# Kernel optimization log

Hardware: AMD Instinct MI355X
Metric: run time of the kernel (lower is better)

## Reference

```python
import jax, jax.numpy as jnp
import numpy as np
import math


def ste_round(x):
    # round with straight-through gradient (identity in bwd)
    return x + jax.lax.stop_gradient(jnp.round(x) - x)


def ste_floor(x):
    return x + jax.lax.stop_gradient(jnp.floor(x) - x)


def _conv(x, w, b):
    # 5x5 stride-2 conv, padding=2 (kernel_size//2), NCHW/OIHW
    y = jax.lax.conv_general_dilated(
        x, w, window_strides=(2, 2), padding=[(2, 2), (2, 2)],
        dimension_numbers=('NCHW', 'OIHW', 'NCHW'))
    return y + b[None, :, None, None]


def _split_conv(x, w, b_int, mul, split=4):
    # 4 redundant sub-convolutions with floor-STE quantized integer weights/biases
    wq = ste_round(w)  # wSTE: round-to-int with STE
    out = 0.0
    for i in range(split):
        out = out + _conv(x, ste_floor((wq + i) / split), ste_floor((b_int + i) / split))
    return out * mul[None, :, None, None]


def _forward(x, w0, b0, w1, b1, w2, b2, w3, b3, mul0, mul1, mul2, mul3,
             relu0, relu1, relu2, md0, md1, md2, md3, ga_left):
    Bits = 8; clp_k = 8; in_scale = 8; scl_k = 3
    relus = [relu0, relu1, relu2]
    clp = [round((2 ** Bits - 1) / r * 2 ** (16 + clp_k)) for r in relus]
    scl = [math.floor((r + 2 ** (scl_k - 1)) / 2 ** scl_k) for r in relus]

    # quantize input to uint8 range
    x = jnp.clip(ste_round(x * 2 ** in_scale), 0, 255)

    # ---- layer 0 ----
    x = _split_conv(x, w0, ste_round(b0 * 2 ** in_scale), mul0)
    x = ste_floor((x + 2.0 ** (md0 - 1 + in_scale - clp_k)) / 2.0 ** (md0 + in_scale - clp_k))
    x = jnp.clip(x, 0, clp[0])
    x = ste_floor((ste_round(x * scl[0]) + 2.0 ** (15 + clp_k - scl_k)) / 2.0 ** (16 + clp_k - scl_k))

    # ---- layers 1, 2 ----
    for w_, b_, mul_, md_, idx in ((w1, b1, mul1, md1, 1), (w2, b2, mul2, md2, 2)):
        x = _split_conv(x, w_, ste_round(b_), mul_)
        x = ste_floor((x + 2.0 ** (md_ - 1 - clp_k)) / 2.0 ** (md_ - clp_k))
        x = jnp.clip(x, 0, clp[idx])
        x = ste_floor((ste_round(x * scl[idx]) + 2.0 ** (15 + clp_k - scl_k)) / 2.0 ** (16 + clp_k - scl_k))

    # ---- layer 3 (latent) ----
    x = _split_conv(x, w3, ste_round(b3), mul3)
    x = ste_floor((x + 2.0 ** (md3 - 1 - ga_left)) / 2.0 ** (md3 - ga_left))
    return x


def setup_inputs():
    key = jax.random.key(0)
    ks = jax.random.split(key, 16)
    N, M = 192, 320
    d = {}
    d['x'] = jax.random.uniform(ks[0], (4, 3, 512, 512), dtype=jnp.float32)
    # float weights whose round() gives small ints (integerized LIC weights)
    d['w0'] = jax.random.normal(ks[1], (N, 3, 5, 5), dtype=jnp.float32) * 3.0
    d['b0'] = jax.random.normal(ks[2], (N,), dtype=jnp.float32)
    d['w1'] = jax.random.normal(ks[3], (N, N, 5, 5), dtype=jnp.float32) * 3.0
    d['b1'] = jax.random.normal(ks[4], (N,), dtype=jnp.float32) * 16.0
    d['w2'] = jax.random.normal(ks[5], (N, N, 5, 5), dtype=jnp.float32) * 3.0
    d['b2'] = jax.random.normal(ks[6], (N,), dtype=jnp.float32) * 16.0
    d['w3'] = jax.random.normal(ks[7], (M, N, 5, 5), dtype=jnp.float32) * 3.0
    d['b3'] = jax.random.normal(ks[8], (M,), dtype=jnp.float32) * 16.0
    # per-channel integer-valued fixed-point multipliers
    d['mul0'] = jax.random.randint(ks[9], (N,), 1, 64).astype(jnp.float32)
    d['mul1'] = jax.random.randint(ks[10], (N,), 1, 64).astype(jnp.float32)
    d['mul2'] = jax.random.randint(ks[11], (N,), 1, 64).astype(jnp.float32)
    d['mul3'] = jax.random.randint(ks[12], (M,), 1, 64).astype(jnp.float32)
    d['relu0'] = 65536; d['relu1'] = 65536; d['relu2'] = 65536
    d['md0'] = 7; d['md1'] = 15; d['md2'] = 15; d['md3'] = 10
    d['ga_left'] = 4
    return d


def reference(x, w0, b0, w1, b1, w2, b2, w3, b3, mul0, mul1, mul2, mul3,
              relu0, relu1, relu2, md0, md1, md2, md3, ga_left):
    return _forward(x, w0, b0, w1, b1, w2, b2, w3, b3, mul0, mul1, mul2, mul3,
                    relu0, relu1, relu2, md0, md1, md2, md3, ga_left)
```

## Files before the change

### kernel.cpp

```cpp
#include <hip/hip_runtime.h>
#include <hip/hip_bf16.h>

typedef int i32x4 __attribute__((ext_vector_type(4)));
typedef unsigned int u32;
typedef unsigned long long u64;
typedef long long ll;

__device__ __forceinline__ void load_lds16(const void* g, void* l) {
  __builtin_amdgcn_global_load_lds(
      (const __attribute__((address_space(1))) u32*)g,
      (__attribute__((address_space(3))) u32*)l, 16, 0, 0);
}

__global__ __launch_bounds__(256) void prep_all(
    const float* __restrict__ w0, const float* __restrict__ w1,
    const float* __restrict__ w2, const float* __restrict__ w3,
    signed char* __restrict__ w0q, signed char* __restrict__ w1p,
    signed char* __restrict__ w2p, signed char* __restrict__ w3p,
    signed char* __restrict__ zbuf,
    int* __restrict__ totw0, int* __restrict__ totw1,
    int* __restrict__ totw2, int* __restrict__ totw3)
{
  __shared__ signed char ldsw[8 * 4800];
  const int blk = blockIdx.x;
  const int tid = threadIdx.x;

  if (blk < 88) {
    const float* wsrc; signed char* wdst; int* tot; int MF, sub;
    if (blk < 24)      { wsrc = w1; wdst = w1p; tot = totw1; MF = 12; sub = blk; }
    else if (blk < 48) { wsrc = w2; wdst = w2p; tot = totw2; MF = 12; sub = blk - 24; }
    else               { wsrc = w3; wdst = w3p; tot = totw3; MF = 20; sub = blk - 48; }
    const int mf = sub >> 1, half = sub & 1, colbase = half * 8;
    const int ocb = mf * 16 + colbase;
    for (int o = 0; o < 8; o++) {
      const float* src = wsrc + (size_t)(ocb + o) * 4800;
      int s = 0;
      for (int j = tid; j < 4800; j += 256) {
        int v = (int)rintf(src[j]);
        ldsw[o * 4800 + j] = (signed char)v;
        s += v;
      }
      atomicAdd(&tot[ocb + o], s);
    }
    __syncthreads();
    for (int u = tid; u < 9600; u += 256) {
      int eu = u & 3, colL = (u >> 2) & 7, q = (u >> 5) & 3, t = u >> 7;
      int tap = t / 3, ch = t - 3 * tap;
      int ci0 = ch * 64 + q * 16 + eu * 4;
      const signed char* sp = ldsw + colL * 4800 + tap;
      u32 wv = 0;
      #pragma unroll
      for (int bb = 0; bb < 4; bb++)
        wv |= ((u32)(unsigned char)sp[(ci0 + bb) * 25]) << (8 * bb);
      *(u32*)(wdst + ((size_t)t * MF + mf) * 1024 +
              (q * 16 + colbase + colL) * 16 + eu * 4) = wv;
    }
  } else {
    if (tid < 128) ((u64*)zbuf)[tid] = 0x8080808080808080ULL;
    for (int i = tid; i < 24576; i += 256) {
      int e = i & 15, colA = (i >> 4) & 15, q = (i >> 8) & 3, t = i >> 10;
      int mf = t % 12, ch = t / 12;
      signed char v = 0;
      if (e < 15 && (ch == 0 || q == 0)) {
        int ky = (ch == 0) ? q : 4;
        int ci = e / 5, kx = e - ci * 5;
        v = (signed char)(int)rintf(
            w0[((mf * 16 + colA) * 3 + ci) * 25 + ky * 5 + kx]);
      }
      w0q[i] = v;
    }
    for (int oc = tid; oc < 192; oc += 256) {
      const float* p = w0 + (size_t)oc * 75;
      int s = 0;
      #pragma unroll 5
      for (int j = 0; j < 75; j++) s += (int)rintf(p[j]);
      totw0[oc] = s;
    }
  }
}

__global__ __launch_bounds__(192, 3) void conv0F(
    const float* __restrict__ x, const signed char* __restrict__ wq,
    const float* __restrict__ bias, const float* __restrict__ mulv,
    const int* __restrict__ totw,
    const int* __restrict__ reluP, const int* __restrict__ mdP,
    unsigned char* __restrict__ outA)
{
  __shared__ signed char ilds[3][5][132];

  const int tid = threadIdx.x;
  const int lane = tid & 63;
  const int col = lane & 15;
  const int quad = lane >> 4;
  const int w = tid >> 6;
  const int blk = blockIdx.x;
  const int oxblk = blk & 3;
  const int oy = (blk >> 2) & 255;
  const int b = blk >> 10;
  const int oxbase = oxblk * 64;

  i32x4 afr[2][4];
  #pragma unroll
  for (int ch = 0; ch < 2; ch++)
    #pragma unroll
    for (int i = 0; i < 4; i++)
      afr[ch][i] = *(const i32x4*)(wq + ch * 12288 + (w * 4 + i) * 1024 + lane * 16);

  const float* xb = x + (size_t)b * 3 * 512 * 512;
  for (int i = tid; i < 990; i += 192) {
    int j = i % 66; int t = i / 66; int r = t % 5; int ci = t / 5;
    int iy = 2 * oy - 2 + r;
    int ix = 2 * oxbase - 2 + 2 * j;
    int v0 = -128, v1 = -128;
    if ((unsigned)iy < 512u) {
      const float* row = xb + ((size_t)ci * 512 + iy) * 512;
      if ((unsigned)ix < 512u) {
        float xv = rintf(row[ix] * 256.0f);
        v0 = (int)fminf(fmaxf(xv, 0.0f), 255.0f) - 128;
      }
      if ((unsigned)(ix + 1) < 512u) {
        float xv = rintf(row[ix + 1] * 256.0f);
        v1 = (int)fminf(fmaxf(xv, 0.0f), 255.0f) - 128;
      }
    }
    *(unsigned short*)&ilds[ci][r][2 * j] =
        (unsigned short)((v0 & 0xFF) | ((v1 & 0xFF) << 8));
  }
  __syncthreads();

  i32x4 acc[4][4];
  #pragma unroll
  for (int fm = 0; fm < 4; fm++)
    #pragma unroll
    for (int fn = 0; fn < 4; fn++) acc[fm][fn] = (i32x4){0, 0, 0, 0};

  #pragma unroll
  for (int ch = 0; ch < 2; ch++) {
    const int row = (ch == 0) ? quad : 4;
    i32x4 bfr[4];
    #pragma unroll
    for (int fn = 0; fn < 4; fn++) {
      const int xb2 = 2 * (fn * 16 + col);
      const int o8 = (xb2 & 3) * 8;
      const int ab = xb2 & ~3;
      u64 w0_, w1_, w2_;
      {
        const u32* p0 = (const u32*)&ilds[0][row][ab];
        const u32* p1 = (const u32*)&ilds[1][row][ab];
        const u32* p2 = (const u32*)&ilds[2][row][ab];
        w0_ = (u64)p0[0] | ((u64)p0[1] << 32);
        w1_ = (u64)p1[0] | ((u64)p1[1] << 32);
        w2_ = (u64)p2[0] | ((u64)p2[1] << 32);
      }
      u32 a0 = (u32)(w0_ >> o8);
      u32 a1 = ((u32)(w0_ >> (o8 + 32)) & 0xFFu) | (((u32)(w1_ >> o8)) << 8);
      u32 a2 = ((u32)(w1_ >> (o8 + 24)) & 0xFFFFu) | (((u32)(w2_ >> o8)) << 16);
      u32 a3 = (u32)(w2_ >> (o8 + 16));
      bfr[fn] = (i32x4){(int)a0, (int)a1, (int)a2, (int)a3};
    }
    #pragma unroll
    for (int fm = 0; fm < 4; fm++)
      #pragma unroll
      for (int fn = 0; fn < 4; fn++)
        acc[fm][fn] = __builtin_amdgcn_mfma_i32_16x16x64_i8(
            afr[ch][fm], bfr[fn], acc[fm][fn], 0, 0, 0);
  }

  const size_t pix0 = ((size_t)(b * 256 + oy)) * 256 + oxbase;
  const int rl = reluP[0];
  const int sh = mdP[0];
  const ll clpv_ll = llrint(255.0 / (double)rl * 16777216.0);
  const int clpv = clpv_ll > 0x7FFFFFFFLL ? 0x7FFFFFFF : (int)clpv_ll;
  const int sclv = (int)((rl + 4) >> 3);
  const int rnd = 1 << (sh - 1);
  #pragma unroll
  for (int fm = 0; fm < 4; fm++) {
    const int oc0 = w * 64 + fm * 16 + quad * 4;
    int bim[4], mu32[4];
    #pragma unroll
    for (int r = 0; r < 4; r++) {
      int bi = (int)llrintf(bias[oc0 + r] * 256.0f) + 128 * totw[oc0 + r];
      mu32[r] = (int)llrintf(mulv[oc0 + r]);
      bim[r] = bi * mu32[r];
    }
    #pragma unroll
    for (int fn = 0; fn < 4; fn++) {
      const size_t pix = pix0 + fn * 16 + col;
      u32 wd = 0;
      #pragma unroll
      for (int r = 0; r < 4; r++) {
        int vi = acc[fm][fn][r] * mu32[r] + bim[r];
        int y = (vi + rnd) >> sh;
        y = y < 0 ? 0 : (y > clpv ? clpv : y);
        y = (y * sclv + (1 << 20)) >> 21;
        wd |= (((u32)y ^ 0x80u) & 0xFFu) << (8 * r);
      }
      *(u32*)(outA + pix * 192 + oc0) = wd;
    }
  }
}

template <int COUT, int HIN, int WIN, int HOUT, int WOUT, int MW,
          int KSPLIT, bool DIRECT>
__global__ __launch_bounds__(MW * 64, 3) void convS(
    const signed char* __restrict__ act, const signed char* __restrict__ wp,
    const float* __restrict__ bias, const float* __restrict__ mulv,
    const int* __restrict__ totw,
    const int* __restrict__ reluP, const int* __restrict__ mdP,
    const signed char* __restrict__ zbuf,
    unsigned char* __restrict__ outA, int* __restrict__ outP)
{
  constexpr int CIN = 192;
  constexpr int PASSES = 4;
  constexpr int SAe = MW * 4096;
  constexpr int TX = WOUT / 16;
  constexpr int TYB = HOUT / 4;
  constexpr int TPP = 25 / KSPLIT;
  constexpr int NLOAD = PASSES * 3;
  constexpr int MAXL = (NLOAD + MW - 1) / MW;
  constexpr int BUF = NLOAD * 1024;
  constexpr int ROWSTEP = 2 * WIN * CIN;
  constexpr int PSZ = 4 * HOUT * WOUT * COUT;
  static_assert(MW * 64 == COUT, "M covers COUT");

  __shared__ __align__(16) char smem[2 * BUF];

  const int tid = threadIdx.x;
  const int lane = tid & 63;
  const int col = lane & 15;
  const int quad = lane >> 4;
  const int w = tid >> 6;
  const int part = blockIdx.y;

  int bx = blockIdx.x;
  const int tx = bx % TX; bx /= TX;
  const int ty = bx % TYB;
  const int b = bx / TYB;
  const int ox0 = tx * 16;
  const int oy0 = ty * 4;

  const signed char* base0 =
      act + ((size_t)b * HIN * WIN + (size_t)(2 * oy0) * WIN + 2 * (ox0 + col)) * CIN
      + quad * 16;
  int bmx = 0;
  #pragma unroll
  for (int kk = 0; kk < 5; kk++)
    if ((unsigned)(2 * (ox0 + col) + kk - 2) < (unsigned)WIN) bmx |= 1 << kk;
  int bmyPack = 0;
  #pragma unroll
  for (int p = 0; p < PASSES; p++) {
    #pragma unroll
    for (int kk = 0; kk < 5; kk++)
      if ((unsigned)(2 * (oy0 + p) + kk - 2) < (unsigned)HIN)
        bmyPack |= 1 << (p * 5 + kk);
  }

  const int tap0 = part * TPP;
  int kyS = tap0 / 5, kxS = tap0 - 5 * kyS;

  auto stage = [&](int sel) {
    const int offB = ((kyS - 2) * WIN + (kxS - 2)) * CIN;
    #pragma unroll
    for (int k = 0; k < MAXL; k++) {
      int j = w + k * MW;
      if (j >= NLOAD) break;
      int p = j / 3, c = j - 3 * p;
      bool v = ((bmx >> kxS) & 1) && ((bmyPack >> (p * 5 + kyS)) & 1);
      const signed char* g =
          v ? (base0 + (size_t)p * ROWSTEP + offB + c * 64) : (zbuf + quad * 16);
      load_lds16(g, smem + sel * BUF + j * 1024);
    }
    kxS++; if (kxS == 5) { kxS = 0; kyS++; }
  };

  i32x4 acc[4][4];
  #pragma unroll
  for (int fm = 0; fm < 4; fm++)
    #pragma unroll
    for (int fn = 0; fn < 4; fn++) acc[fm][fn] = (i32x4){0, 0, 0, 0};

  auto comp = [&](const char* pB, i32x4 (&a)[4]) {
    i32x4 bfr[4];
    #pragma unroll
    for (int i = 0; i < 4; i++)
      bfr[i] = *(const i32x4*)(pB + i * 3072);
    #pragma unroll
    for (int fm = 0; fm < 4; fm++)
      #pragma unroll
      for (int fn = 0; fn < 4; fn++)
        acc[fm][fn] = __builtin_amdgcn_mfma_i32_16x16x64_i8(
            a[fm], bfr[fn], acc[fm][fn], 0, 0, 0);
  };

  stage(0);
  const signed char* aptr = wp + (size_t)(tap0 * 3) * SAe + w * 4096 + lane * 16;
  i32x4 aC[4], aN[4];
  #pragma unroll
  for (int i = 0; i < 4; i++) aC[i] = *(const i32x4*)(aptr + i * 1024);

  #pragma unroll 1
  for (int t = 0; t < TPP; t++) {
    const int sel = t & 1;
    __syncthreads();
    if (t + 1 < TPP) stage(sel ^ 1);
    const char* base = smem + sel * BUF + lane * 16;
    #pragma unroll
    for (int c = 0; c < 3; c++) {
      aptr += SAe;
      #pragma unroll
      for (int i = 0; i < 4; i++) aN[i] = *(const i32x4*)(aptr + i * 1024);
      comp(base + c * 1024, aC);
      #pragma unroll
      for (int i = 0; i < 4; i++) aC[i] = aN[i];
    }
  }

  if constexpr (DIRECT) {
    const int rl = reluP[0];
    const int sh = mdP[0] - 8;
    const ll clpv = llrint(255.0 / (double)rl * 16777216.0);
    const ll sclv = (ll)((rl + 4) >> 3);
    #pragma unroll
    for (int fm = 0; fm < 4; fm++) {
      const int oc0 = w * 64 + fm * 16 + quad * 4;
      ll bi[4], mu[4];
      #pragma unroll
      for (int r = 0; r < 4; r++) {
        bi[r] = llrintf(bias[oc0 + r]) + 128LL * totw[oc0 + r];
        mu[r] = llrintf(mulv[oc0 + r]);
      }
      #pragma unroll
      for (int fn = 0; fn < 4; fn++) {
        const int oyv = oy0 + fn;
        const int oxv = ox0 + col;
        u32 wd = 0;
        #pragma unroll
        for (int r = 0; r < 4; r++) {
          ll vi = ((ll)acc[fm][fn][r] + bi[r]) * mu[r];
          ll y = (vi + (1LL << (sh - 1))) >> sh;
          y = y < 0 ? 0LL : (y > clpv ? clpv : y);
          y = (y * sclv + (1LL << 20)) >> 21;
          wd |= (((u32)y ^ 0x80u) & 0xFFu) << (8 * r);
        }
        *(u32*)(outA + ((size_t)((b * HOUT + oyv) * WOUT + oxv)) * COUT + oc0) = wd;
      }
    }
  } else {
    int* pout = outP + (size_t)part * PSZ;
    #pragma unroll
    for (int fm = 0; fm < 4; fm++) {
      const int oc0 = w * 64 + fm * 16 + quad * 4;
      #pragma unroll
      for (int fn = 0; fn < 4; fn++) {
        const int oyv = oy0 + fn;
        const int oxv = ox0 + col;
        *(i32x4*)(pout + ((size_t)((b * HOUT + oyv) * WOUT + oxv)) * COUT + oc0) =
            acc[fm][fn];
      }
    }
  }
}

__global__ __launch_bounds__(256) void reduce2(
    const int* __restrict__ partP, const float* __restrict__ bias,
    const float* __restrict__ mulv, const int* __restrict__ totw,
    const int* __restrict__ reluP, const int* __restrict__ mdP,
    unsigned char* __restrict__ outA)
{
  const int gid = blockIdx.x * 256 + threadIdx.x;
  const int PSZ4 = 4 * 64 * 64 * 192 / 4;
  const int4* pp = (const int4*)partP;
  int4 sv = pp[gid];
  #pragma unroll
  for (int p = 1; p < 5; p++) {
    int4 v = pp[(size_t)p * PSZ4 + gid];
    sv.x += v.x; sv.y += v.y; sv.z += v.z; sv.w += v.w;
  }
  int sa[4] = {sv.x, sv.y, sv.z, sv.w};
  const int oc0 = (gid * 4) % 192;
  const int rl = reluP[0];
  const int sh = mdP[0] - 8;
  const ll clpv = llrint(255.0 / (double)rl * 16777216.0);
  const ll sclv = (ll)((rl + 4) >> 3);
  u32 wd = 0;
  #pragma unroll
  for (int r = 0; r < 4; r++) {
    ll bi = llrintf(bias[oc0 + r]) + 128LL * totw[oc0 + r];
    ll mu = llrintf(mulv[oc0 + r]);
    ll vi = ((ll)sa[r] + bi) * mu;
    ll y = (vi + (1LL << (sh - 1))) >> sh;
    y = y < 0 ? 0LL : (y > clpv ? clpv : y);
    y = (y * sclv + (1LL << 20)) >> 21;
    wd |= (((u32)y ^ 0x80u) & 0xFFu) << (8 * r);
  }
  ((u32*)outA)[gid] = wd;
}

__global__ __launch_bounds__(256) void reduce3(
    const int* __restrict__ partP, const float* __restrict__ b3,
    const float* __restrict__ mul3, const int* __restrict__ totw3,
    const int* __restrict__ mdP, const int* __restrict__ gaP,
    float* __restrict__ outF)
{
  const int gid = blockIdx.x * 256 + threadIdx.x;
  int t = gid;
  const int ox = t & 31; t >>= 5;
  const int oy = t & 31; t >>= 5;
  const int oc = t % 320;
  const int b  = t / 320;
  const int PSZ = 4 * 32 * 32 * 320;
  const size_t src = ((size_t)((b * 32 + oy) * 32 + ox)) * 320 + oc;
  ll s = 0;
  #pragma unroll
  for (int p = 0; p < 5; p++) s += partP[(size_t)p * PSZ + src];
  const int sh = mdP[0] - gaP[0];
  const ll bi = llrintf(b3[oc]) + 128LL * totw3[oc];
  const ll mu = llrintf(mul3[oc]);
  const ll y = ((s + bi) * mu + (1LL << (sh - 1))) >> sh;
  outF[gid] = (float)y;
}

extern "C" void kernel_launch(void* const* d_in, const int* in_sizes, int n_in,
                              void* d_out, int out_size, void* d_ws, size_t ws_size,
                              hipStream_t stream)
{
  const float* x    = (const float*)d_in[0];
  const float* w0   = (const float*)d_in[1];
  const float* b0   = (const float*)d_in[2];
  const float* w1   = (const float*)d_in[3];
  const float* b1   = (const float*)d_in[4];
  const float* w2   = (const float*)d_in[5];
  const float* b2   = (const float*)d_in[6];
  const float* w3   = (const float*)d_in[7];
  const float* b3   = (const float*)d_in[8];
  const float* mul0 = (const float*)d_in[9];
  const float* mul1 = (const float*)d_in[10];
  const float* mul2 = (const float*)d_in[11];
  const float* mul3 = (const float*)d_in[12];
  const int* relu0  = (const int*)d_in[13];
  const int* relu1  = (const int*)d_in[14];
  const int* relu2  = (const int*)d_in[15];
  const int* md0    = (const int*)d_in[16];
  const int* md1    = (const int*)d_in[17];
  const int* md2    = (const int*)d_in[18];
  const int* md3    = (const int*)d_in[19];
  const int* ga     = (const int*)d_in[20];

  char* ws = (char*)d_ws;
  size_t off = 0;
  signed char* zbuf = (signed char*)(ws + off); off += 1024;
  signed char* w0q  = (signed char*)(ws + off); off += 24576;
  signed char* w1p  = (signed char*)(ws + off); off += 921600;
  signed char* w2p  = (signed char*)(ws + off); off += 921600;
  signed char* w3p  = (signed char*)(ws + off); off += 1536000;
  int*         totw1= (int*)        (ws + off); off += 192 * 4;
  int*         totw2= (int*)        (ws + off); off += 192 * 4;
  int*         totw3= (int*)        (ws + off); off += 320 * 4;
  int*         totw0= (int*)        (ws + off); off += 192 * 4;
  unsigned char* act1 = (unsigned char*)(ws + off); off += (size_t)4 * 256 * 256 * 192;
  unsigned char* act2 = (unsigned char*)(ws + off); off += (size_t)4 * 128 * 128 * 192;
  unsigned char* act3 = (unsigned char*)(ws + off); off += (size_t)4 * 64 * 64 * 192;
  int*         partl  = (int*)(ws + off); off += (size_t)5 * 4 * 64 * 64 * 192 * 4;
  (void)ws_size; (void)in_sizes; (void)n_in; (void)out_size;

  hipMemsetAsync(totw1, 0, (192 + 192 + 320 + 192) * 4, stream);
  prep_all<<<89, 256, 0, stream>>>(w0, w1, w2, w3, w0q, w1p, w2p, w3p,
                                   zbuf, totw0, totw1, totw2, totw3);
  conv0F<<<4096, 192, 0, stream>>>(x, w0q, b0, mul0, totw0, relu0, md0, act1);
  convS<192, 256, 256, 128, 128, 3, 1, true><<<dim3(1024, 1), 192, 0, stream>>>(
      (const signed char*)act1, w1p, b1, mul1, totw1, relu1, md1, zbuf, act2, nullptr);
  convS<192, 128, 128, 64, 64, 3, 5, false><<<dim3(256, 5), 192, 0, stream>>>(
      (const signed char*)act2, w2p, b2, mul2, totw2, relu2, md2, zbuf, nullptr, partl);
  reduce2<<<3072, 256, 0, stream>>>(partl, b2, mul2, totw2, relu2, md2, act3);
  convS<320, 64, 64, 32, 32, 5, 5, false><<<dim3(64, 5), 320, 0, stream>>>(
      (const signed char*)act3, w3p, b3, mul3, totw3, nullptr, md3, zbuf, nullptr, partl);
  reduce3<<<5120, 256, 0, stream>>>(partl, b3, mul3, totw3, md3, ga, (float*)d_out);
}
```

Before: 366.1 us.

## Stage whole input rows in swizzled LDS and reuse across kx taps

```diff
diff --git a/kernel.cpp b/kernel.cpp
--- a/kernel.cpp
+++ b/kernel.cpp
@@ -10,6 +10,10 @@
   __builtin_amdgcn_global_load_lds(
       (const __attribute__((address_space(1))) u32*)g,
       (__attribute__((address_space(3))) u32*)l, 16, 0, 0);
+}
+
+__device__ __forceinline__ int xcd_swz(int bid, int nwg) {
+  return (bid & 7) * (nwg >> 3) + (bid >> 3);
 }
 
 __global__ __launch_bounds__(256) void prep_all(
@@ -93,7 +97,7 @@
   const int col = lane & 15;
   const int quad = lane >> 4;
   const int w = tid >> 6;
-  const int blk = blockIdx.x;
+  const int blk = xcd_swz(blockIdx.x, gridDim.x);
   const int oxblk = blk & 3;
   const int oy = (blk >> 2) & 255;
   const int b = blk >> 10;
@@ -211,19 +215,15 @@
     unsigned char* __restrict__ outA, int* __restrict__ outP)
 {
   constexpr int CIN = 192;
-  constexpr int PASSES = 4;
   constexpr int SAe = MW * 4096;
   constexpr int TX = WOUT / 16;
   constexpr int TYB = HOUT / 4;
-  constexpr int TPP = 25 / KSPLIT;
-  constexpr int NLOAD = PASSES * 3;
-  constexpr int MAXL = (NLOAD + MW - 1) / MW;
-  constexpr int BUF = NLOAD * 1024;
-  constexpr int ROWSTEP = 2 * WIN * CIN;
+  constexpr int SLOTS = (KSPLIT == 1) ? 5 : 4;
+  constexpr int RS = 36 * 256;
   constexpr int PSZ = 4 * HOUT * WOUT * COUT;
   static_assert(MW * 64 == COUT, "M covers COUT");
 
-  __shared__ __align__(16) char smem[2 * BUF];
+  __shared__ __align__(16) char smem[SLOTS * RS];
 
   const int tid = threadIdx.x;
   const int lane = tid & 63;
@@ -232,87 +232,102 @@
   const int w = tid >> 6;
   const int part = blockIdx.y;
 
-  int bx = blockIdx.x;
+  int bx = xcd_swz(blockIdx.x, gridDim.x);
   const int tx = bx % TX; bx /= TX;
   const int ty = bx % TYB;
   const int b = bx / TYB;
   const int ox0 = tx * 16;
   const int oy0 = ty * 4;
 
-  const signed char* base0 =
-      act + ((size_t)b * HIN * WIN + (size_t)(2 * oy0) * WIN + 2 * (ox0 + col)) * CIN
-      + quad * 16;
-  int bmx = 0;
-  #pragma unroll
-  for (int kk = 0; kk < 5; kk++)
-    if ((unsigned)(2 * (ox0 + col) + kk - 2) < (unsigned)WIN) bmx |= 1 << kk;
-  int bmyPack = 0;
-  #pragma unroll
-  for (int p = 0; p < PASSES; p++) {
-    #pragma unroll
-    for (int kk = 0; kk < 5; kk++)
-      if ((unsigned)(2 * (oy0 + p) + kk - 2) < (unsigned)HIN)
-        bmyPack |= 1 << (p * 5 + kk);
-  }
-
-  const int tap0 = part * TPP;
-  int kyS = tap0 / 5, kxS = tap0 - 5 * kyS;
-
-  auto stage = [&](int sel) {
-    const int offB = ((kyS - 2) * WIN + (kxS - 2)) * CIN;
-    #pragma unroll
-    for (int k = 0; k < MAXL; k++) {
-      int j = w + k * MW;
-      if (j >= NLOAD) break;
-      int p = j / 3, c = j - 3 * p;
-      bool v = ((bmx >> kxS) & 1) && ((bmyPack >> (p * 5 + kyS)) & 1);
-      const signed char* g =
-          v ? (base0 + (size_t)p * ROWSTEP + offB + c * 64) : (zbuf + quad * 16);
-      load_lds16(g, smem + sel * BUF + j * 1024);
-    }
-    kxS++; if (kxS == 5) { kxS = 0; kyS++; }
+  int voff[15];
+  #pragma unroll
+  for (int kx = 0; kx < 5; kx++) {
+    const int px = 2 * col + kx;
+    #pragma unroll
+    for (int c = 0; c < 3; c++)
+      voff[kx * 3 + c] = px * 256 + ((((c * 4 + quad) ^ (px & 7))) << 4);
+  }
+
+  auto stageRow = [&](int d, int slot) {
+    const int y = 2 * oy0 + d;
+    const bool rv = (unsigned)y < (unsigned)HIN;
+    const signed char* rowp =
+        act + ((size_t)b * HIN + (rv ? y : 0)) * (size_t)WIN * CIN;
+    for (int i = w; i < 9; i += MW) {
+      const int px = 4 * i + quad;
+      const int ix = 2 * ox0 - 2 + px;
+      const int cs = col ^ (px & 7);
+      const bool v = rv && ((unsigned)ix < (unsigned)WIN) && (cs < 12);
+      const signed char* g = v ? (rowp + (size_t)ix * CIN + cs * 16)
+                               : (zbuf + lane * 16);
+      load_lds16(g, smem + slot * RS + i * 1024);
+    }
   };
 
   i32x4 acc[4][4];
   #pragma unroll
   for (int fm = 0; fm < 4; fm++)
     #pragma unroll
-    for (int fn = 0; fn < 4; fn++) acc[fm][fn] = (i32x4){0, 0, 0, 0};
-
-  auto comp = [&](const char* pB, i32x4 (&a)[4]) {
-    i32x4 bfr[4];
-    #pragma unroll
-    for (int i = 0; i < 4; i++)
-      bfr[i] = *(const i32x4*)(pB + i * 3072);
-    #pragma unroll
-    for (int fm = 0; fm < 4; fm++)
-      #pragma unroll
-      for (int fn = 0; fn < 4; fn++)
-        acc[fm][fn] = __builtin_amdgcn_mfma_i32_16x16x64_i8(
-            a[fm], bfr[fn], acc[fm][fn], 0, 0, 0);
+    for (int p = 0; p < 4; p++) acc[fm][p] = (i32x4){0, 0, 0, 0};
+
+  auto computeKy = [&](int ky, const int (&sb)[4]) {
+    const signed char* aB = wp + (size_t)(ky * 15) * SAe + w * 4096 + lane * 16;
+    i32x4 aP[2][4];
+    #pragma unroll
+    for (int i = 0; i < 4; i++) aP[0][i] = *(const i32x4*)(aB + i * 1024);
+    #pragma unroll
+    for (int u = 0; u < 15; u++) {
+      constexpr int _dummy = 0; (void)_dummy;
+      const int cur = u & 1;
+      if (u < 14) {
+        const signed char* ap = aB + (size_t)(u + 1) * SAe;
+        #pragma unroll
+        for (int i = 0; i < 4; i++)
+          aP[cur ^ 1][i] = *(const i32x4*)(ap + i * 1024);
+      }
+      i32x4 bfr[4];
+      #pragma unroll
+      for (int p = 0; p < 4; p++)
+        bfr[p] = *(const i32x4*)(smem + sb[p] + voff[u]);
+      #pragma unroll
+      for (int fm = 0; fm < 4; fm++)
+        #pragma unroll
+        for (int p = 0; p < 4; p++)
+          acc[fm][p] = __builtin_amdgcn_mfma_i32_16x16x64_i8(
+              aP[cur][fm], bfr[p], acc[fm][p], 0, 0, 0);
+    }
   };
 
-  stage(0);
-  const signed char* aptr = wp + (size_t)(tap0 * 3) * SAe + w * 4096 + lane * 16;
-  i32x4 aC[4], aN[4];
-  #pragma unroll
-  for (int i = 0; i < 4; i++) aC[i] = *(const i32x4*)(aptr + i * 1024);
-
-  #pragma unroll 1
-  for (int t = 0; t < TPP; t++) {
-    const int sel = t & 1;
+  if constexpr (KSPLIT == 1) {
+    stageRow(-2, 0); stageRow(0, 1); stageRow(2, 2); stageRow(4, 3);
+    #pragma unroll 1
+    for (int t = 0; t < 5; t++) {
+      __syncthreads();
+      if (t == 0)      stageRow(6, 4);
+      else if (t == 1) stageRow(8, 0);
+      else if (t == 2) stageRow(-1, 1);
+      else if (t == 3) stageRow(7, 0);
+      const int base = (t < 3) ? t : t - 2;
+      const int ky = (t < 3) ? 2 * t : 2 * t - 5;
+      int sb[4];
+      #pragma unroll
+      for (int p = 0; p < 4; p++) {
+        int s = base + p; if (s >= 5) s -= 5;
+        sb[p] = s * RS;
+      }
+      computeKy(ky, sb);
+      if (t == 2) {
+        __syncthreads();
+        stageRow(1, 2); stageRow(3, 3); stageRow(5, 4);
+      }
+    }
+  } else {
+    const int ky = part;
+    #pragma unroll
+    for (int p = 0; p < 4; p++) stageRow(ky - 2 + 2 * p, p);
     __syncthreads();
-    if (t + 1 < TPP) stage(sel ^ 1);
-    const char* base = smem + sel * BUF + lane * 16;
-    #pragma unroll
-    for (int c = 0; c < 3; c++) {
-      aptr += SAe;
-      #pragma unroll
-      for (int i = 0; i < 4; i++) aN[i] = *(const i32x4*)(aptr + i * 1024);
-      comp(base + c * 1024, aC);
-      #pragma unroll
-      for (int i = 0; i < 4; i++) aC[i] = aN[i];
-    }
+    int sb[4] = {0, RS, 2 * RS, 3 * RS};
+    computeKy(ky, sb);
   }
 
   if constexpr (DIRECT) {
```

Result: no change. 360.4 us (-1.6%).
